# Performance work log

Hardware: AMD Instinct MI355X
Metric: run time of the kernel (lower is better)

Reference implementation:

```python
import jax, jax.numpy as jnp
import numpy as np

# Dims
B, S, D = 2, 2048, 1024
H, KV = 16, 4            # rosa heads / kv heads -> n_rep = 4
QKB, VB = 16, 32          # query-key bits / value bits
N_REP = H // KV
TAU = 1.0


def setup_inputs() -> dict:
    key = jax.random.key(0)
    ks = jax.random.split(key, 8)
    sc = lambda fan_in: 1.0 / np.sqrt(fan_in)
    return {
        "hidden_states": jax.random.normal(ks[0], (B, S, D), jnp.float32),
        # Linear weights stored (in, out) so y = x @ W
        "Wq": jax.random.normal(ks[1], (D, H * QKB), jnp.float32) * sc(D),
        "Wk": jax.random.normal(ks[2], (D, KV * QKB), jnp.float32) * sc(D),
        "Wv": jax.random.normal(ks[3], (D, KV * VB), jnp.float32) * sc(D),
        "Wo": jax.random.normal(ks[4], (H * VB, D), jnp.float32) * sc(H * VB),
        "v_emb0": jnp.full((H * VB,), -1e-05, jnp.float32),
        "v_emb1": jnp.full((H * VB,), +1e-05, jnp.float32),
    }


def _repeat_kv(x, n_rep):
    # x: [B, KV, S, d] -> [B, KV*n_rep, S, d]
    b, kv, s, d = x.shape
    return jnp.broadcast_to(x[:, :, None], (b, kv, n_rep, s, d)).reshape(b, kv * n_rep, s, d)


def reference(hidden_states, Wq, Wk, Wv, Wo, v_emb0, v_emb1):
    b, s, _ = hidden_states.shape
    q = (hidden_states @ Wq).reshape(b, s, H, QKB).transpose(0, 2, 1, 3)   # [B,H,S,QKB]
    k = (hidden_states @ Wk).reshape(b, s, KV, QKB).transpose(0, 2, 1, 3)
    v = (hidden_states @ Wv).reshape(b, s, KV, VB).transpose(0, 2, 1, 3)
    k = _repeat_kv(k, N_REP)                                               # [B,H,S,QKB]
    v = _repeat_kv(v, N_REP)                                               # [B,H,S,VB]

    # Soft binarization (hard path uses (x > 0); soft path relaxes with sigmoid(x/tau)).
    pq = jax.nn.sigmoid(q / TAU)
    pk = jax.nn.sigmoid(k / TAU)
    pv = jax.nn.sigmoid(v / TAU)

    # Expected number of matching bits between soft-binary q_i and k_j:
    # sum_b [ pq*pk + (1-pq)(1-pk) ] = QKB - sum(pq) - sum(pk) + 2 * pq.pk
    dot = jnp.einsum("bhsd,bhtd->bhst", pq, pk)                            # [B,H,S,S]
    scores = QKB - pq.sum(-1)[:, :, :, None] - pk.sum(-1)[:, :, None, :] + 2.0 * dot

    causal = jnp.tril(jnp.ones((s, s), bool))                              # [S,S]
    scores = jnp.where(causal[None, None], scores, jnp.finfo(scores.dtype).min)
    attn = jax.nn.softmax(scores / TAU, axis=-1)

    vh = jnp.einsum("bhst,bhtd->bhsd", attn, pv)                           # [B,H,S,VB]
    e0 = v_emb0.reshape(1, H, 1, VB)
    e1 = v_emb1.reshape(1, H, 1, VB)
    out = e0 * (1.0 - vh) + e1 * vh                                        # [B,H,S,VB]
    out = out.transpose(0, 2, 1, 3).reshape(b, s, H * VB)
    return out @ Wo                                                        # [B,S,D]
```

## Files before the change

kernel.cpp:

```cpp
#include <hip/hip_runtime.h>
#include <hip/hip_bf16.h>

#define B_    2
#define S_    2048
#define D_    1024
#define H_    16
#define KV_   4
#define QKB_  16
#define VB_   32
#define NTOK  (B_ * S_)
#define L2E_  1.44269504088896f

typedef __attribute__((ext_vector_type(8))) short bshort8;
typedef __attribute__((ext_vector_type(4))) float f32x4;

__device__ __forceinline__ unsigned short bf16_rne(float x) {
    unsigned u = __float_as_uint(x);
    return (unsigned short)((u + 0x7FFFu + ((u >> 16) & 1u)) >> 16);
}
__device__ __forceinline__ unsigned bf16x2_rne(float lo, float hi) {
    return (unsigned)bf16_rne(lo) | ((unsigned)bf16_rne(hi) << 16);
}
__device__ __forceinline__ float sum2bf(unsigned u) {
    return __uint_as_float(u << 16) + __uint_as_float(u & 0xFFFF0000u);
}
__device__ __forceinline__ void stage16(const unsigned short* g, unsigned short* l) {
    __builtin_amdgcn_global_load_lds(
        (const __attribute__((address_space(1))) void*)g,
        (__attribute__((address_space(3))) void*)l, 16, 0, 0);
}

__global__ __launch_bounds__(256) void prep_kernel(
    const float* __restrict__ hs,
    const float* __restrict__ Wq, const float* __restrict__ Wk,
    const float* __restrict__ Wv, const float* __restrict__ Wo,
    unsigned short* __restrict__ hs_b,
    unsigned short* __restrict__ Wcat_t, unsigned short* __restrict__ Wot)
{
    __shared__ float T[64][65];
    const int t = threadIdx.x;
    if (blockIdx.x < 2048) {
        int i = blockIdx.x * 256 + t;
        const float4* s = (const float4*)hs;
        float4 a = s[2 * i], b = s[2 * i + 1];
        uint4 o;
        o.x = bf16x2_rne(a.x, a.y); o.y = bf16x2_rne(a.z, a.w);
        o.z = bf16x2_rne(b.x, b.y); o.w = bf16x2_rne(b.z, b.w);
        ((uint4*)hs_b)[i] = o;
        return;
    }
    const int bid = blockIdx.x - 2048;
    const float* src; unsigned short* dst; int K, N, tk, tn, drow0;
    if (bid < 64)       { src = Wq; dst = Wcat_t; K = 1024; N = 256;  int r = bid;       tk = r & 15; tn = r >> 4; drow0 = 0; }
    else if (bid < 80)  { src = Wk; dst = Wcat_t; K = 1024; N = 64;   int r = bid - 64;  tk = r;      tn = 0;      drow0 = 256; }
    else if (bid < 112) { src = Wv; dst = Wcat_t; K = 1024; N = 128;  int r = bid - 80;  tk = r & 15; tn = r >> 4; drow0 = 320; }
    else                { src = Wo; dst = Wot;    K = 512;  N = 1024; int r = bid - 112; tk = r & 7;  tn = r >> 3; drow0 = 0; }
    const int k0 = tk * 64, n0 = tn * 64;
    const int rr = t >> 4, cc = (t & 15) * 4;
    #pragma unroll
    for (int i = 0; i < 4; ++i) {
        float4 v = *(const float4*)(src + (k0 + rr + i * 16) * N + n0 + cc);
        T[rr + i * 16][cc + 0] = v.x; T[rr + i * 16][cc + 1] = v.y;
        T[rr + i * 16][cc + 2] = v.z; T[rr + i * 16][cc + 3] = v.w;
    }
    __syncthreads();
    const int nloc = t >> 2, kc = (t & 3) * 16;
    unsigned o[8];
    #pragma unroll
    for (int j = 0; j < 8; ++j)
        o[j] = bf16x2_rne(T[kc + 2 * j][nloc], T[kc + 2 * j + 1][nloc]);
    unsigned short* dp = dst + (drow0 + n0 + nloc) * K + k0 + kc;
    uint4 w0; w0.x = o[0]; w0.y = o[1]; w0.z = o[2]; w0.w = o[3];
    uint4 w1; w1.x = o[4]; w1.y = o[5]; w1.z = o[6]; w1.w = o[7];
    *(uint4*)(dp) = w0;
    *(uint4*)(dp + 8) = w1;
}

__global__ __launch_bounds__(256, 4) void proj_gemm(
    const unsigned short* __restrict__ Ab, const unsigned short* __restrict__ Btb,
    unsigned short* __restrict__ qg, unsigned short* __restrict__ pko,
    unsigned short* __restrict__ pvT)
{
    __shared__ unsigned short As[64 * 64];
    __shared__ unsigned short Bs[64 * 64];
    const int tid = threadIdx.x, l = tid & 63, w = tid >> 6;
    const int l15 = l & 15, quad = l >> 4;
    const int m0 = blockIdx.x * 64, n0 = blockIdx.y * 64;
    const int sr8 = l >> 3, sc8 = l & 7;
    f32x4 c[4];
    #pragma unroll
    for (int j = 0; j < 4; ++j) c[j] = (f32x4){0.f, 0.f, 0.f, 0.f};

    for (int k0 = 0; k0 < 1024; k0 += 64) {
        int R0 = w * 8, r0 = R0 + sr8;
        int R1 = 32 + w * 8, r1 = R1 + sr8;
        stage16(Ab  + (m0 + r0) * 1024 + k0 + (sc8 ^ (r0 & 7)) * 8, &As[R0 * 64]);
        stage16(Ab  + (m0 + r1) * 1024 + k0 + (sc8 ^ (r1 & 7)) * 8, &As[R1 * 64]);
        stage16(Btb + (n0 + r0) * 1024 + k0 + (sc8 ^ (r0 & 7)) * 8, &Bs[R0 * 64]);
        stage16(Btb + (n0 + r1) * 1024 + k0 + (sc8 ^ (r1 & 7)) * 8, &Bs[R1 * 64]);
        __syncthreads();
        #pragma unroll
        for (int kh = 0; kh < 2; ++kh) {
            const int arow = w * 16 + l15;
            bshort8 a = *(const bshort8*)&As[arow * 64 + (((kh * 4 + quad) ^ (arow & 7)) * 8)];
            #pragma unroll
            for (int bc = 0; bc < 4; ++bc) {
                const int brow = bc * 16 + l15;
                bshort8 b = *(const bshort8*)&Bs[brow * 64 + (((kh * 4 + quad) ^ (brow & 7)) * 8)];
                c[bc] = __builtin_amdgcn_mfma_f32_16x16x32_bf16(a, b, c[bc], 0, 0, 0);
            }
        }
        __syncthreads();
    }

    const int tok0 = m0 + w * 16 + quad * 4;
    #pragma unroll
    for (int bc = 0; bc < 4; ++bc) {
        f32x4 v = c[bc];
        const int n = n0 + bc * 16 + l15;
        float sg[4];
        #pragma unroll
        for (int r = 0; r < 4; ++r)
            sg[r] = 1.f / (1.f + exp2f(-v[r] * L2E_));
        if (n < 256) {
            const int hh = n >> 4, d = n & 15;
            #pragma unroll
            for (int r = 0; r < 4; ++r) {
                int tok = tok0 + r, bb = tok >> 11, ss = tok & 2047;
                qg[(((bb * 16 + hh) * 2048) + ss) * 16 + d] =
                    bf16_rne(L2E_ * (2.f * sg[r] - 1.f));
            }
        } else if (n < 320) {
            const int j = n - 256, kvv = j >> 4, d = j & 15;
            #pragma unroll
            for (int r = 0; r < 4; ++r) {
                int tok = tok0 + r, bb = tok >> 11, ss = tok & 2047;
                pko[(((bb * 4 + kvv) * 2048) + ss) * 16 + d] = bf16_rne(sg[r]);
            }
        } else {
            const int j = n - 320, kvv = j >> 5, d = j & 31;
            const int bb = tok0 >> 11, ss = tok0 & 2047;
            const int tl = ss >> 6, ccol = ss & 63;
            uint2 wv; wv.x = bf16x2_rne(sg[0], sg[1]); wv.y = bf16x2_rne(sg[2], sg[3]);
            *(uint2*)(pvT + ((((bb * 4 + kvv) * 32) + tl) * 32 + d) * 64 + ccol) = wv;
        }
    }
}

__global__ __launch_bounds__(256, 2) void outproj_gemm(
    const unsigned short* __restrict__ Ab, const unsigned short* __restrict__ Btb,
    float* __restrict__ out)
{
    __shared__ unsigned short As[64 * 64];
    __shared__ unsigned short Bs[128 * 64];
    const int tid = threadIdx.x, l = tid & 63, w = tid >> 6;
    const int l15 = l & 15, quad = l >> 4;
    const int m0 = blockIdx.x * 64, n0 = blockIdx.y * 128;
    const int wr = w & 1, wc = w >> 1;
    const int sr8 = l >> 3, sc8 = l & 7;
    f32x4 c[2][4];
    #pragma unroll
    for (int i = 0; i < 2; ++i)
        #pragma unroll
        for (int j = 0; j < 4; ++j) c[i][j] = (f32x4){0.f, 0.f, 0.f, 0.f};

    for (int k0 = 0; k0 < 512; k0 += 64) {
        #pragma unroll
        for (int j = 0; j < 2; ++j) {
            int R = w * 16 + j * 8, r = R + sr8;
            stage16(Ab + (m0 + r) * 512 + k0 + (sc8 ^ (r & 7)) * 8, &As[R * 64]);
        }
        #pragma unroll
        for (int j = 0; j < 4; ++j) {
            int R = j * 32 + w * 8, r = R + sr8;
            stage16(Btb + (n0 + r) * 512 + k0 + (sc8 ^ (r & 7)) * 8, &Bs[R * 64]);
        }
        __syncthreads();
        #pragma unroll
        for (int kh = 0; kh < 2; ++kh) {
            bshort8 a[2], b[4];
            #pragma unroll
            for (int ar = 0; ar < 2; ++ar) {
                int row = wr * 32 + ar * 16 + l15;
                a[ar] = *(const bshort8*)&As[row * 64 + (((kh * 4 + quad) ^ (row & 7)) * 8)];
            }
            #pragma unroll
            for (int bc = 0; bc < 4; ++bc) {
                int row = wc * 64 + bc * 16 + l15;
                b[bc] = *(const bshort8*)&Bs[row * 64 + (((kh * 4 + quad) ^ (row & 7)) * 8)];
            }
            #pragma unroll
            for (int ar = 0; ar < 2; ++ar)
                #pragma unroll
                for (int bc = 0; bc < 4; ++bc)
                    c[ar][bc] = __builtin_amdgcn_mfma_f32_16x16x32_bf16(a[ar], b[bc], c[ar][bc], 0, 0, 0);
        }
        __syncthreads();
    }

    #pragma unroll
    for (int ar = 0; ar < 2; ++ar)
        #pragma unroll
        for (int bc = 0; bc < 4; ++bc) {
            f32x4 v = c[ar][bc];
            const int col = n0 + wc * 64 + bc * 16 + l15;
            const int r0 = m0 + wr * 32 + ar * 16 + quad * 4;
            #pragma unroll
            for (int r = 0; r < 4; ++r)
                out[(r0 + r) * D_ + col] = v[r];
        }
}

__global__ __launch_bounds__(256, 4) void attn_kernel(
    const unsigned short* __restrict__ qg_g, const unsigned short* __restrict__ pk_g,
    const unsigned short* __restrict__ pvT_g, const float* __restrict__ e0,
    const float* __restrict__ e1, unsigned short* __restrict__ xo)
{
    __shared__ unsigned short P[4][16][88];
    const int tid = threadIdx.x, l = tid & 63, wq = tid >> 6;
    const int l15 = l & 15, quad = l >> 4;
    const int g = blockIdx.x;
    const int idx = g & 255, kg = g >> 8;
    const int bh = idx & 31, rr = idx >> 5;
    int qt;
    if      (kg == 0) qt = rr;
    else if (kg == 1) qt = 31 - rr;
    else if (kg == 2) qt = 8 + rr;
    else              qt = 23 - rr;
    const int b = bh >> 4, h = bh & 15, kv = h >> 2;
    const int qbase = qt * 64;
    const unsigned short* pkb = pk_g + ((b * 4 + kv) * 2048) * 16;
    const unsigned short* pvb = pvT_g + (b * 4 + kv) * 65536;
    const unsigned short* qgb = qg_g + ((b * 16 + h) * 2048) * 16;

    const f32x4 zero4 = {0.f, 0.f, 0.f, 0.f};
    const bshort8 zero8 = {0, 0, 0, 0, 0, 0, 0, 0};

    const unsigned short* qrow = qgb + (qbase + wq * 16 + l15) * 16;
    uint4 qu0 = *(const uint4*)qrow;
    uint4 qu1 = *(const uint4*)(qrow + 8);
    float s = sum2bf(qu0.x) + sum2bf(qu0.y) + sum2bf(qu0.z) + sum2bf(qu0.w)
            + sum2bf(qu1.x) + sum2bf(qu1.y) + sum2bf(qu1.z) + sum2bf(qu1.w);
    bshort8 qfrag = zero8;
    if (quad == 0)      qfrag = __builtin_bit_cast(bshort8, qu0);
    else if (quad == 1) qfrag = __builtin_bit_cast(bshort8, qu1);
    else if (quad == 2) qfrag[0] = (short)bf16_rne(-8.f * L2E_ - 0.5f * s);

    bshort8 kone = zero8; kone[0] = (short)0x3F80;

    f32x4 acc0 = zero4, acc1 = zero4;
    float lsum = 0.f;

    bshort8 kc[4], vc[4], kn[4], vn[4];
    if (quad < 2) {
        #pragma unroll
        for (int ks = 0; ks < 4; ++ks)
            kc[ks] = *(const bshort8*)(pkb + (ks * 16 + l15) * 16 + quad * 8);
    }
    {
        const unsigned short* vb = pvb + l15 * 64 + quad * 8;
        vc[0] = *(const bshort8*)(vb);
        vc[1] = *(const bshort8*)(vb + 32);
        vc[2] = *(const bshort8*)(vb + 1024);
        vc[3] = *(const bshort8*)(vb + 1056);
    }

    #pragma unroll 2
    for (int t = 0; t < qt; ++t) {
        if (quad < 2) {
            #pragma unroll
            for (int ks = 0; ks < 4; ++ks)
                kn[ks] = *(const bshort8*)(pkb + ((t + 1) * 64 + ks * 16 + l15) * 16 + quad * 8);
        }
        {
            const unsigned short* vb = pvb + (t + 1) * 2048 + l15 * 64 + quad * 8;
            vn[0] = *(const bshort8*)(vb);
            vn[1] = *(const bshort8*)(vb + 32);
            vn[2] = *(const bshort8*)(vb + 1024);
            vn[3] = *(const bshort8*)(vb + 1056);
        }
        f32x4 sc[4];
        #pragma unroll
        for (int ks = 0; ks < 4; ++ks) {
            bshort8 kf;
            if (quad < 2)       kf = kc[ks];
            else if (quad == 2) kf = kone;
            else                kf = zero8;
            sc[ks] = __builtin_amdgcn_mfma_f32_16x16x32_bf16(kf, qfrag, zero4, 0, 0, 0);
        }
        #pragma unroll
        for (int ks = 0; ks < 4; ++ks) {
            float p0 = exp2f(sc[ks][0]), p1 = exp2f(sc[ks][1]);
            float p2 = exp2f(sc[ks][2]), p3 = exp2f(sc[ks][3]);
            lsum += p0 + p1 + p2 + p3;
            uint2 wv; wv.x = bf16x2_rne(p0, p1); wv.y = bf16x2_rne(p2, p3);
            *(uint2*)&P[wq][l15][ks * 16 + quad * 4] = wv;
        }
        {
            bshort8 pf0 = *(const bshort8*)&P[wq][l15][quad * 8];
            bshort8 pf1 = *(const bshort8*)&P[wq][l15][32 + quad * 8];
            acc0 = __builtin_amdgcn_mfma_f32_16x16x32_bf16(vc[0], pf0, acc0, 0, 0, 0);
            acc1 = __builtin_amdgcn_mfma_f32_16x16x32_bf16(vc[2], pf0, acc1, 0, 0, 0);
            acc0 = __builtin_amdgcn_mfma_f32_16x16x32_bf16(vc[1], pf1, acc0, 0, 0, 0);
            acc1 = __builtin_amdgcn_mfma_f32_16x16x32_bf16(vc[3], pf1, acc1, 0, 0, 0);
        }
        #pragma unroll
        for (int i = 0; i < 4; ++i) { kc[i] = kn[i]; vc[i] = vn[i]; }
    }

    {
        const int t0 = qt * 64;
        const int q_lane = qbase + wq * 16 + l15;
        f32x4 sc[4];
        #pragma unroll
        for (int ks = 0; ks < 4; ++ks) {
            bshort8 kf;
            if (quad < 2)       kf = kc[ks];
            else if (quad == 2) kf = kone;
            else                kf = zero8;
            sc[ks] = __builtin_amdgcn_mfma_f32_16x16x32_bf16(kf, qfrag, zero4, 0, 0, 0);
        }
        #pragma unroll
        for (int ks = 0; ks < 4; ++ks) {
            float pv0[4];
            #pragma unroll
            for (int r = 0; r < 4; ++r) {
                const int tg = t0 + ks * 16 + quad * 4 + r;
                float pp = (tg <= q_lane) ? exp2f(sc[ks][r]) : 0.f;
                lsum += pp; pv0[r] = pp;
            }
            uint2 wv; wv.x = bf16x2_rne(pv0[0], pv0[1]); wv.y = bf16x2_rne(pv0[2], pv0[3]);
            *(uint2*)&P[wq][l15][ks * 16 + quad * 4] = wv;
        }
        {
            bshort8 pf0 = *(const bshort8*)&P[wq][l15][quad * 8];
            bshort8 pf1 = *(const bshort8*)&P[wq][l15][32 + quad * 8];
            acc0 = __builtin_amdgcn_mfma_f32_16x16x32_bf16(vc[0], pf0, acc0, 0, 0, 0);
            acc1 = __builtin_amdgcn_mfma_f32_16x16x32_bf16(vc[2], pf0, acc1, 0, 0, 0);
            acc0 = __builtin_amdgcn_mfma_f32_16x16x32_bf16(vc[1], pf1, acc0, 0, 0, 0);
            acc1 = __builtin_amdgcn_mfma_f32_16x16x32_bf16(vc[3], pf1, acc1, 0, 0, 0);
        }
    }

    lsum += __shfl_xor(lsum, 16);
    lsum += __shfl_xor(lsum, 32);
    const float inv = 1.f / lsum;

    float e0v[8], dEv[8];
    #pragma unroll
    for (int vs = 0; vs < 2; ++vs)
        #pragma unroll
        for (int r = 0; r < 4; ++r) {
            int idx2 = h * 32 + vs * 16 + quad * 4 + r;
            float a = e0[idx2];
            e0v[vs * 4 + r] = a; dEv[vs * 4 + r] = e1[idx2] - a;
        }
    const int tok = b * 2048 + qbase + wq * 16 + l15;
    float o0[4], o1[4];
    #pragma unroll
    for (int r = 0; r < 4; ++r) {
        o0[r] = e0v[r]     + dEv[r]     * (acc0[r] * inv);
        o1[r] = e0v[4 + r] + dEv[4 + r] * (acc1[r] * inv);
    }
    uint2 w0; w0.x = bf16x2_rne(o0[0], o0[1]); w0.y = bf16x2_rne(o0[2], o0[3]);
    uint2 w1; w1.x = bf16x2_rne(o1[0], o1[1]); w1.y = bf16x2_rne(o1[2], o1[3]);
    *(uint2*)(xo + tok * 512 + h * 32 + quad * 4)      = w0;
    *(uint2*)(xo + tok * 512 + h * 32 + 16 + quad * 4) = w1;
}

extern "C" void kernel_launch(void* const* d_in, const int* in_sizes, int n_in,
                              void* d_out, int out_size, void* d_ws, size_t ws_size,
                              hipStream_t stream)
{
    const float* hs = (const float*)d_in[0];
    const float* Wq = (const float*)d_in[1];
    const float* Wk = (const float*)d_in[2];
    const float* Wv = (const float*)d_in[3];
    const float* Wo = (const float*)d_in[4];
    const float* e0 = (const float*)d_in[5];
    const float* e1 = (const float*)d_in[6];
    float* out = (float*)d_out;

    char* ws = (char*)d_ws;
    unsigned short* hs_b   = (unsigned short*)(ws);
    unsigned short* xo     = (unsigned short*)(ws);
    unsigned short* Wcat_t = (unsigned short*)(ws + 8388608);
    unsigned short* Wot    = (unsigned short*)(ws + 8388608 + 917504);
    unsigned short* qg     = (unsigned short*)(ws + 10354688);
    unsigned short* pk     = (unsigned short*)(ws + 12451840);
    unsigned short* pvT    = (unsigned short*)(ws + 12976128);

    prep_kernel<<<2288, 256, 0, stream>>>(hs, Wq, Wk, Wv, Wo, hs_b, Wcat_t, Wot);
    proj_gemm<<<dim3(64, 7), 256, 0, stream>>>(hs_b, Wcat_t, qg, pk, pvT);
    attn_kernel<<<1024, 256, 0, stream>>>(qg, pk, pvT, e0, e1, xo);
    outproj_gemm<<<dim3(64, 8), 256, 0, stream>>>(xo, Wot, out);
}
```

Before: 145.7 us.

## Rebalance causal attention with paired short/long query tiles split across two waves

The attention kernel now uses 128-thread blocks of two waves. Each block pairs a short query tile pp with its mirror 31-pp, giving every block the same amount of causal work. Wave 0 handles the whole short tile plus the first part of the long tile's keys. Wave 1 handles the rest of the long tile, and the two partial accumulators and softmax sums are merged through shared memory before the write. Software bf16 rounding is also replaced with the hardware v_cvt_pk_bf16_f32 instruction, which cuts ALU work in the exp/convert loop but may change rounding slightly.

```diff
diff --git a/kernel.cpp b/kernel.cpp
--- a/kernel.cpp
+++ b/kernel.cpp
@@ -20,6 +20,11 @@
 }
 __device__ __forceinline__ unsigned bf16x2_rne(float lo, float hi) {
     return (unsigned)bf16_rne(lo) | ((unsigned)bf16_rne(hi) << 16);
+}
+__device__ __forceinline__ unsigned cvt_pk_bf16(float lo, float hi) {
+    unsigned r;
+    asm("v_cvt_pk_bf16_f32 %0, %1, %2" : "=v"(r) : "v"(lo), "v"(hi));
+    return r;
 }
 __device__ __forceinline__ float sum2bf(unsigned u) {
     return __uint_as_float(u << 16) + __uint_as_float(u & 0xFFFF0000u);
@@ -211,75 +216,55 @@
         }
 }
 
-__global__ __launch_bounds__(256, 4) void attn_kernel(
+__global__ __launch_bounds__(128, 4) void attn_kernel(
     const unsigned short* __restrict__ qg_g, const unsigned short* __restrict__ pk_g,
     const unsigned short* __restrict__ pvT_g, const float* __restrict__ e0,
     const float* __restrict__ e1, unsigned short* __restrict__ xo)
 {
-    __shared__ unsigned short P[4][16][88];
-    const int tid = threadIdx.x, l = tid & 63, wq = tid >> 6;
+    __shared__ unsigned short P[2][16][72];
+    __shared__ float CMB[9][64];
+    const int tid = threadIdx.x, l = tid & 63, w = tid >> 6;
     const int l15 = l & 15, quad = l >> 4;
     const int g = blockIdx.x;
-    const int idx = g & 255, kg = g >> 8;
-    const int bh = idx & 31, rr = idx >> 5;
-    int qt;
-    if      (kg == 0) qt = rr;
-    else if (kg == 1) qt = 31 - rr;
-    else if (kg == 2) qt = 8 + rr;
-    else              qt = 23 - rr;
+    const int bh = g & 31, pp = (g >> 5) & 15, slot = g >> 9;
     const int b = bh >> 4, h = bh & 15, kv = h >> 2;
-    const int qbase = qt * 64;
+    const int q31 = 31 - pp;
     const unsigned short* pkb = pk_g + ((b * 4 + kv) * 2048) * 16;
     const unsigned short* pvb = pvT_g + (b * 4 + kv) * 65536;
     const unsigned short* qgb = qg_g + ((b * 16 + h) * 2048) * 16;
 
     const f32x4 zero4 = {0.f, 0.f, 0.f, 0.f};
     const bshort8 zero8 = {0, 0, 0, 0, 0, 0, 0, 0};
-
-    const unsigned short* qrow = qgb + (qbase + wq * 16 + l15) * 16;
-    uint4 qu0 = *(const uint4*)qrow;
-    uint4 qu1 = *(const uint4*)(qrow + 8);
-    float s = sum2bf(qu0.x) + sum2bf(qu0.y) + sum2bf(qu0.z) + sum2bf(qu0.w)
-            + sum2bf(qu1.x) + sum2bf(qu1.y) + sum2bf(qu1.z) + sum2bf(qu1.w);
-    bshort8 qfrag = zero8;
-    if (quad == 0)      qfrag = __builtin_bit_cast(bshort8, qu0);
-    else if (quad == 1) qfrag = __builtin_bit_cast(bshort8, qu1);
-    else if (quad == 2) qfrag[0] = (short)bf16_rne(-8.f * L2E_ - 0.5f * s);
-
     bshort8 kone = zero8; kone[0] = (short)0x3F80;
 
-    f32x4 acc0 = zero4, acc1 = zero4;
-    float lsum = 0.f;
-
-    bshort8 kc[4], vc[4], kn[4], vn[4];
-    if (quad < 2) {
-        #pragma unroll
-        for (int ks = 0; ks < 4; ++ks)
-            kc[ks] = *(const bshort8*)(pkb + (ks * 16 + l15) * 16 + quad * 8);
-    }
-    {
-        const unsigned short* vb = pvb + l15 * 64 + quad * 8;
-        vc[0] = *(const bshort8*)(vb);
-        vc[1] = *(const bshort8*)(vb + 32);
-        vc[2] = *(const bshort8*)(vb + 1024);
-        vc[3] = *(const bshort8*)(vb + 1056);
-    }
-
-    #pragma unroll 2
-    for (int t = 0; t < qt; ++t) {
+    f32x4 acc0, acc1; float lsum;
+    bshort8 qfrag;
+    bshort8 kc[4], vc[4];
+
+    auto loadQ = [&](int T) {
+        const unsigned short* qrow = qgb + (T * 64 + slot * 16 + l15) * 16;
+        uint4 qu0 = *(const uint4*)qrow;
+        uint4 qu1 = *(const uint4*)(qrow + 8);
+        float s = sum2bf(qu0.x) + sum2bf(qu0.y) + sum2bf(qu0.z) + sum2bf(qu0.w)
+                + sum2bf(qu1.x) + sum2bf(qu1.y) + sum2bf(qu1.z) + sum2bf(qu1.w);
+        qfrag = zero8;
+        if (quad == 0)      qfrag = __builtin_bit_cast(bshort8, qu0);
+        else if (quad == 1) qfrag = __builtin_bit_cast(bshort8, qu1);
+        else if (quad == 2) qfrag[0] = (short)bf16_rne(-8.f * L2E_ - 0.5f * s);
+    };
+    auto loadKV = [&](int t, bshort8* kk, bshort8* vv) {
         if (quad < 2) {
             #pragma unroll
             for (int ks = 0; ks < 4; ++ks)
-                kn[ks] = *(const bshort8*)(pkb + ((t + 1) * 64 + ks * 16 + l15) * 16 + quad * 8);
-        }
-        {
-            const unsigned short* vb = pvb + (t + 1) * 2048 + l15 * 64 + quad * 8;
-            vn[0] = *(const bshort8*)(vb);
-            vn[1] = *(const bshort8*)(vb + 32);
-            vn[2] = *(const bshort8*)(vb + 1024);
-            vn[3] = *(const bshort8*)(vb + 1056);
-        }
-        f32x4 sc[4];
+                kk[ks] = *(const bshort8*)(pkb + (t * 64 + ks * 16 + l15) * 16 + quad * 8);
+        }
+        const unsigned short* vb = pvb + t * 2048 + l15 * 64 + quad * 8;
+        vv[0] = *(const bshort8*)(vb);
+        vv[1] = *(const bshort8*)(vb + 32);
+        vv[2] = *(const bshort8*)(vb + 1024);
+        vv[3] = *(const bshort8*)(vb + 1056);
+    };
+    auto qk = [&](f32x4* sc) {
         #pragma unroll
         for (int ks = 0; ks < 4; ++ks) {
             bshort8 kf;
@@ -288,84 +273,103 @@
             else                kf = zero8;
             sc[ks] = __builtin_amdgcn_mfma_f32_16x16x32_bf16(kf, qfrag, zero4, 0, 0, 0);
         }
-        #pragma unroll
-        for (int ks = 0; ks < 4; ++ks) {
-            float p0 = exp2f(sc[ks][0]), p1 = exp2f(sc[ks][1]);
-            float p2 = exp2f(sc[ks][2]), p3 = exp2f(sc[ks][3]);
-            lsum += p0 + p1 + p2 + p3;
-            uint2 wv; wv.x = bf16x2_rne(p0, p1); wv.y = bf16x2_rne(p2, p3);
-            *(uint2*)&P[wq][l15][ks * 16 + quad * 4] = wv;
-        }
-        {
-            bshort8 pf0 = *(const bshort8*)&P[wq][l15][quad * 8];
-            bshort8 pf1 = *(const bshort8*)&P[wq][l15][32 + quad * 8];
-            acc0 = __builtin_amdgcn_mfma_f32_16x16x32_bf16(vc[0], pf0, acc0, 0, 0, 0);
-            acc1 = __builtin_amdgcn_mfma_f32_16x16x32_bf16(vc[2], pf0, acc1, 0, 0, 0);
-            acc0 = __builtin_amdgcn_mfma_f32_16x16x32_bf16(vc[1], pf1, acc0, 0, 0, 0);
-            acc1 = __builtin_amdgcn_mfma_f32_16x16x32_bf16(vc[3], pf1, acc1, 0, 0, 0);
-        }
-        #pragma unroll
-        for (int i = 0; i < 4; ++i) { kc[i] = kn[i]; vc[i] = vn[i]; }
-    }
-
-    {
-        const int t0 = qt * 64;
-        const int q_lane = qbase + wq * 16 + l15;
-        f32x4 sc[4];
-        #pragma unroll
-        for (int ks = 0; ks < 4; ++ks) {
-            bshort8 kf;
-            if (quad < 2)       kf = kc[ks];
-            else if (quad == 2) kf = kone;
-            else                kf = zero8;
-            sc[ks] = __builtin_amdgcn_mfma_f32_16x16x32_bf16(kf, qfrag, zero4, 0, 0, 0);
-        }
-        #pragma unroll
-        for (int ks = 0; ks < 4; ++ks) {
-            float pv0[4];
+    };
+    auto pv = [&]() {
+        bshort8 pf0 = *(const bshort8*)&P[w][l15][quad * 8];
+        bshort8 pf1 = *(const bshort8*)&P[w][l15][32 + quad * 8];
+        acc0 = __builtin_amdgcn_mfma_f32_16x16x32_bf16(vc[0], pf0, acc0, 0, 0, 0);
+        acc1 = __builtin_amdgcn_mfma_f32_16x16x32_bf16(vc[2], pf0, acc1, 0, 0, 0);
+        acc0 = __builtin_amdgcn_mfma_f32_16x16x32_bf16(vc[1], pf1, acc0, 0, 0, 0);
+        acc1 = __builtin_amdgcn_mfma_f32_16x16x32_bf16(vc[3], pf1, acc1, 0, 0, 0);
+    };
+
+    auto segment = [&](int T, int kt0, int nfull, bool peel) {
+        acc0 = zero4; acc1 = zero4; lsum = 0.f;
+        loadKV(kt0, kc, vc);
+        bshort8 kn[4], vn[4];
+        #pragma unroll 2
+        for (int t = 0; t < nfull; ++t) {
+            loadKV(kt0 + t + 1, kn, vn);
+            f32x4 sc[4]; qk(sc);
+            #pragma unroll
+            for (int ks = 0; ks < 4; ++ks) {
+                float p0 = exp2f(sc[ks][0]), p1 = exp2f(sc[ks][1]);
+                float p2 = exp2f(sc[ks][2]), p3 = exp2f(sc[ks][3]);
+                lsum += p0 + p1 + p2 + p3;
+                uint2 wv; wv.x = cvt_pk_bf16(p0, p1); wv.y = cvt_pk_bf16(p2, p3);
+                *(uint2*)&P[w][l15][ks * 16 + quad * 4] = wv;
+            }
+            pv();
+            #pragma unroll
+            for (int i = 0; i < 4; ++i) { kc[i] = kn[i]; vc[i] = vn[i]; }
+        }
+        if (peel) {
+            const int t0 = T * 64;
+            const int q_lane = T * 64 + slot * 16 + l15;
+            f32x4 sc[4]; qk(sc);
+            #pragma unroll
+            for (int ks = 0; ks < 4; ++ks) {
+                float pvx[4];
+                #pragma unroll
+                for (int r = 0; r < 4; ++r) {
+                    const int tg = t0 + ks * 16 + quad * 4 + r;
+                    float ppv = (tg <= q_lane) ? exp2f(sc[ks][r]) : 0.f;
+                    lsum += ppv; pvx[r] = ppv;
+                }
+                uint2 wv; wv.x = cvt_pk_bf16(pvx[0], pvx[1]); wv.y = cvt_pk_bf16(pvx[2], pvx[3]);
+                *(uint2*)&P[w][l15][ks * 16 + quad * 4] = wv;
+            }
+            pv();
+        }
+    };
+
+    auto writeout = [&](int T) {
+        float ls = lsum;
+        ls += __shfl_xor(ls, 16);
+        ls += __shfl_xor(ls, 32);
+        const float inv = 1.f / ls;
+        float e0v[8], dEv[8];
+        #pragma unroll
+        for (int vs = 0; vs < 2; ++vs)
             #pragma unroll
             for (int r = 0; r < 4; ++r) {
-                const int tg = t0 + ks * 16 + quad * 4 + r;
-                float pp = (tg <= q_lane) ? exp2f(sc[ks][r]) : 0.f;
-                lsum += pp; pv0[r] = pp;
-            }
-            uint2 wv; wv.x = bf16x2_rne(pv0[0], pv0[1]); wv.y = bf16x2_rne(pv0[2], pv0[3]);
-            *(uint2*)&P[wq][l15][ks * 16 + quad * 4] = wv;
-        }
-        {
-            bshort8 pf0 = *(const bshort8*)&P[wq][l15][quad * 8];
-            bshort8 pf1 = *(const bshort8*)&P[wq][l15][32 + quad * 8];
-            acc0 = __builtin_amdgcn_mfma_f32_16x16x32_bf16(vc[0], pf0, acc0, 0, 0, 0);
-            acc1 = __builtin_amdgcn_mfma_f32_16x16x32_bf16(vc[2], pf0, acc1, 0, 0, 0);
-            acc0 = __builtin_amdgcn_mfma_f32_16x16x32_bf16(vc[1], pf1, acc0, 0, 0, 0);
-            acc1 = __builtin_amdgcn_mfma_f32_16x16x32_bf16(vc[3], pf1, acc1, 0, 0, 0);
-        }
-    }
-
-    lsum += __shfl_xor(lsum, 16);
-    lsum += __shfl_xor(lsum, 32);
-    const float inv = 1.f / lsum;
-
-    float e0v[8], dEv[8];
-    #pragma unroll
-    for (int vs = 0; vs < 2; ++vs)
+                int idx2 = h * 32 + vs * 16 + quad * 4 + r;
+                float a = e0[idx2];
+                e0v[vs * 4 + r] = a; dEv[vs * 4 + r] = e1[idx2] - a;
+            }
+        const int tok = b * 2048 + T * 64 + slot * 16 + l15;
+        float o0[4], o1[4];
         #pragma unroll
         for (int r = 0; r < 4; ++r) {
-            int idx2 = h * 32 + vs * 16 + quad * 4 + r;
-            float a = e0[idx2];
-            e0v[vs * 4 + r] = a; dEv[vs * 4 + r] = e1[idx2] - a;
-        }
-    const int tok = b * 2048 + qbase + wq * 16 + l15;
-    float o0[4], o1[4];
-    #pragma unroll
-    for (int r = 0; r < 4; ++r) {
-        o0[r] = e0v[r]     + dEv[r]     * (acc0[r] * inv);
-        o1[r] = e0v[4 + r] + dEv[4 + r] * (acc1[r] * inv);
-    }
-    uint2 w0; w0.x = bf16x2_rne(o0[0], o0[1]); w0.y = bf16x2_rne(o0[2], o0[3]);
-    uint2 w1; w1.x = bf16x2_rne(o1[0], o1[1]); w1.y = bf16x2_rne(o1[2], o1[3]);
-    *(uint2*)(xo + tok * 512 + h * 32 + quad * 4)      = w0;
-    *(uint2*)(xo + tok * 512 + h * 32 + 16 + quad * 4) = w1;
+            o0[r] = e0v[r]     + dEv[r]     * (acc0[r] * inv);
+            o1[r] = e0v[4 + r] + dEv[4 + r] * (acc1[r] * inv);
+        }
+        uint2 w0, w1;
+        w0.x = cvt_pk_bf16(o0[0], o0[1]); w0.y = cvt_pk_bf16(o0[2], o0[3]);
+        w1.x = cvt_pk_bf16(o1[0], o1[1]); w1.y = cvt_pk_bf16(o1[2], o1[3]);
+        *(uint2*)(xo + tok * 512 + h * 32 + quad * 4)      = w0;
+        *(uint2*)(xo + tok * 512 + h * 32 + 16 + quad * 4) = w1;
+    };
+
+    if (w == 0) {
+        loadQ(pp);
+        segment(pp, 0, pp, true);
+        writeout(pp);
+        loadQ(q31);
+        segment(q31, 0, 16 - pp, false);
+        CMB[0][l] = acc0[0]; CMB[1][l] = acc0[1]; CMB[2][l] = acc0[2]; CMB[3][l] = acc0[3];
+        CMB[4][l] = acc1[0]; CMB[5][l] = acc1[1]; CMB[6][l] = acc1[2]; CMB[7][l] = acc1[3];
+        CMB[8][l] = lsum;
+        __syncthreads();
+    } else {
+        loadQ(q31);
+        segment(q31, 16 - pp, 15, true);
+        __syncthreads();
+        acc0[0] += CMB[0][l]; acc0[1] += CMB[1][l]; acc0[2] += CMB[2][l]; acc0[3] += CMB[3][l];
+        acc1[0] += CMB[4][l]; acc1[1] += CMB[5][l]; acc1[2] += CMB[6][l]; acc1[3] += CMB[7][l];
+        lsum += CMB[8][l];
+        writeout(q31);
+    }
 }
 
 extern "C" void kernel_launch(void* const* d_in, const int* in_sizes, int n_in,
@@ -392,6 +396,6 @@
 
     prep_kernel<<<2288, 256, 0, stream>>>(hs, Wq, Wk, Wv, Wo, hs_b, Wcat_t, Wot);
     proj_gemm<<<dim3(64, 7), 256, 0, stream>>>(hs_b, Wcat_t, qg, pk, pvT);
-    attn_kernel<<<1024, 256, 0, stream>>>(qg, pk, pvT, e0, e1, xo);
+    attn_kernel<<<2048, 128, 0, stream>>>(qg, pk, pvT, e0, e1, xo);
     outproj_gemm<<<dim3(64, 8), 256, 0, stream>>>(xo, Wot, out);
 }
```

Result: slower. 189.4 us (+30.0%).
